# Kernel optimization log

Hardware: AMD Instinct MI355X
Metric: run time of the kernel (lower is better)

## Reference

```python
import jax, jax.numpy as jnp
import numpy as np
from jax import lax

D = 768; H = 8; DQ = D // H; NL = 6; FF = 3072; MAXREL = 100; NOUT = 1024
B = 8; T = 4096; CIN = 8
EPS = 1e-5
NREL = 2 * MAXREL - 1  # 199 learned relative positions, rel in [-99, 99]


def conv1d(x, w, b, stride=1, pad=1):
    # x [B,C,T], w [O,I,K]
    y = lax.conv_general_dilated(x, w, (stride,), [(pad, pad)],
                                 dimension_numbers=('NCH', 'OIH', 'NCH'))
    return y + b[None, :, None]


def bnorm(x, p):
    # eval-mode BatchNorm1d; p [4,C] = (gamma, beta, running_mean, running_var)
    g, be, m, v = p[0], p[1], p[2], p[3]
    return g[None, :, None] * (x - m[None, :, None]) * lax.rsqrt(v[None, :, None] + EPS) + be[None, :, None]


def resblock(x, c1w, c1b, b1, c2w, c2b, b2, rw, rb, br):
    h = jax.nn.relu(bnorm(conv1d(x, c1w, c1b, stride=2), b1))
    h = bnorm(conv1d(h, c2w, c2b), b2)
    res = bnorm(conv1d(x, rw, rb, stride=2, pad=0), br)
    return jax.nn.relu(h + res)


def layer_norm(x, g, b):
    mu = jnp.mean(x, axis=-1, keepdims=True)
    var = jnp.mean(jnp.square(x - mu), axis=-1, keepdims=True)
    return g * (x - mu) * lax.rsqrt(var + EPS) + b


def attention(x, wq, wk, wv, wo, rel):
    # x [B,L,D]; wq/wk/wv [H,D,DQ]; wo [H,DQ,D]; rel [H,NREL,DQ]
    L = x.shape[1]
    q = jnp.einsum('bld,hdk->bhlk', x, wq)
    k = jnp.einsum('bld,hdk->bhlk', x, wk)
    v = jnp.einsum('bld,hdk->bhlk', x, wv)
    logits = jnp.einsum('bhqk,bhmk->bhqm', q, k) / np.float32(np.sqrt(DQ))
    # relative positional logits: pos[b,h,i,j] = q[b,h,i] . rel[h, (j-i)+99] if |j-i|<100 else -1e8
    rel_logits = jnp.einsum('bhlk,hmk->bhlm', q, rel)  # [B,H,L,NREL]
    pos_idx = jnp.arange(L)[None, :] - jnp.arange(L)[:, None] + (MAXREL - 1)  # j - i + 99
    valid = (pos_idx >= 0) & (pos_idx < NREL)
    idxc = jnp.clip(pos_idx, 0, NREL - 1)
    pos = jnp.take_along_axis(rel_logits, idxc[None, None, :, :], axis=3)  # [B,H,L,L]
    logits = logits + jnp.where(valid[None, None], pos, jnp.float32(-1e8))
    probs = jax.nn.softmax(logits, axis=-1)
    o = jnp.einsum('bhqm,bhmk->bhqk', probs, v)
    return jnp.einsum('bhlk,hkd->bld', o, wo)


def forward(x_raw, rb1_c1w, rb1_c1b, rb1_bn1, rb1_c2w, rb1_c2b, rb1_bn2, rb1_rw, rb1_rb, rb1_bnr,
            rb23_c1w, rb23_c1b, rb23_bn1, rb23_c2w, rb23_c2b, rb23_bn2, rb23_rw, rb23_rb, rb23_bnr,
            w_in_w, w_in_b, wq, wk, wv, wo, rel_emb, ln1_g, ln1_b, ln2_g, ln2_b,
            ff1_w, ff1_b, ff2_w, ff2_b, w_out_w, w_out_b):
    x = jnp.transpose(x_raw, (0, 2, 1))  # [B, 8, T]
    x = resblock(x, rb1_c1w, rb1_c1b, rb1_bn1, rb1_c2w, rb1_c2b, rb1_bn2, rb1_rw, rb1_rb, rb1_bnr)
    for i in range(2):
        x = resblock(x, rb23_c1w[i], rb23_c1b[i], rb23_bn1[i], rb23_c2w[i], rb23_c2b[i],
                     rb23_bn2[i], rb23_rw[i], rb23_rb[i], rb23_bnr[i])
    x = jnp.transpose(x, (0, 2, 1))  # [B, L=T/8, D]
    x = x @ w_in_w.T + w_in_b
    for l in range(NL):  # post-norm transformer encoder layers
        x = layer_norm(x + attention(x, wq[l], wk[l], wv[l], wo[l], rel_emb[l]), ln1_g[l], ln1_b[l])
        h = jax.nn.relu(x @ ff1_w[l].T + ff1_b[l]) @ ff2_w[l].T + ff2_b[l]
        x = layer_norm(x + h, ln2_g[l], ln2_b[l])
    return x @ w_out_w.T + w_out_b


def setup_inputs() -> dict:
    key = jax.random.key(0)
    ks = iter(jax.random.split(key, 128))

    def w(shape, scale):
        return jax.random.normal(next(ks), shape, dtype=jnp.float32) * scale

    def bnp(*lead):
        g = 1.0 + 0.1 * jax.random.normal(next(ks), (*lead, D), dtype=jnp.float32)
        be = 0.1 * jax.random.normal(next(ks), (*lead, D), dtype=jnp.float32)
        m = 0.1 * jax.random.normal(next(ks), (*lead, D), dtype=jnp.float32)
        v = jax.random.uniform(next(ks), (*lead, D), minval=0.5, maxval=1.5, dtype=jnp.float32)
        return jnp.stack([g, be, m, v], axis=-2)  # [..., 4, D]

    inp = {}
    inp['x_raw'] = jax.random.normal(next(ks), (B, T, CIN), dtype=jnp.float32)
    inp['rb1_c1w'] = w((D, CIN, 3), 0.2); inp['rb1_c1b'] = w((D,), 0.02); inp['rb1_bn1'] = bnp()
    inp['rb1_c2w'] = w((D, D, 3), 0.02); inp['rb1_c2b'] = w((D,), 0.02); inp['rb1_bn2'] = bnp()
    inp['rb1_rw'] = w((D, CIN, 1), 0.2); inp['rb1_rb'] = w((D,), 0.02); inp['rb1_bnr'] = bnp()
    inp['rb23_c1w'] = w((2, D, D, 3), 0.02); inp['rb23_c1b'] = w((2, D), 0.02); inp['rb23_bn1'] = bnp(2)
    inp['rb23_c2w'] = w((2, D, D, 3), 0.02); inp['rb23_c2b'] = w((2, D), 0.02); inp['rb23_bn2'] = bnp(2)
    inp['rb23_rw'] = w((2, D, D, 1), 0.02); inp['rb23_rb'] = w((2, D), 0.02); inp['rb23_bnr'] = bnp(2)
    inp['w_in_w'] = w((D, D), 0.02); inp['w_in_b'] = w((D,), 0.02)
    sd = D ** -0.5
    inp['wq'] = w((NL, H, D, DQ), sd); inp['wk'] = w((NL, H, D, DQ), sd)
    inp['wv'] = w((NL, H, D, DQ), sd); inp['wo'] = w((NL, H, DQ, D), sd)
    inp['rel_emb'] = w((NL, H, NREL, DQ), DQ ** -0.5)
    inp['ln1_g'] = jnp.ones((NL, D), jnp.float32); inp['ln1_b'] = jnp.zeros((NL, D), jnp.float32)
    inp['ln2_g'] = jnp.ones((NL, D), jnp.float32); inp['ln2_b'] = jnp.zeros((NL, D), jnp.float32)
    inp['ff1_w'] = w((NL, FF, D), 0.02); inp['ff1_b'] = w((NL, FF), 0.02)
    inp['ff2_w'] = w((NL, D, FF), 0.02); inp['ff2_b'] = w((NL, D), 0.02)
    inp['w_out_w'] = w((NOUT, D), 0.02); inp['w_out_b'] = w((NOUT,), 0.02)
    return inp


def reference(x_raw, rb1_c1w, rb1_c1b, rb1_bn1, rb1_c2w, rb1_c2b, rb1_bn2, rb1_rw, rb1_rb, rb1_bnr,
              rb23_c1w, rb23_c1b, rb23_bn1, rb23_c2w, rb23_c2b, rb23_bn2, rb23_rw, rb23_rb, rb23_bnr,
              w_in_w, w_in_b, wq, wk, wv, wo, rel_emb, ln1_g, ln1_b, ln2_g, ln2_b,
              ff1_w, ff1_b, ff2_w, ff2_b, w_out_w, w_out_b):
    return forward(x_raw, rb1_c1w, rb1_c1b, rb1_bn1, rb1_c2w, rb1_c2b, rb1_bn2, rb1_rw, rb1_rb, rb1_bnr,
                   rb23_c1w, rb23_c1b, rb23_bn1, rb23_c2w, rb23_c2b, rb23_bn2, rb23_rw, rb23_rb, rb23_bnr,
                   w_in_w, w_in_b, wq, wk, wv, wo, rel_emb, ln1_g, ln1_b, ln2_g, ln2_b,
                   ff1_w, ff1_b, ff2_w, ff2_b, w_out_w, w_out_b)
```

## Files before the change

### kernel.cpp

```cpp
#include <hip/hip_runtime.h>
#include <math.h>

typedef __bf16 bf16;
typedef bf16 bf16x8 __attribute__((ext_vector_type(8)));
typedef bf16 bf16x4 __attribute__((ext_vector_type(4)));
typedef float f32x4 __attribute__((ext_vector_type(4)));
#define EPSF 1e-5f

__device__ __forceinline__ void ldg_lds16(const bf16* g, bf16* l) {
    __builtin_amdgcn_global_load_lds((const __attribute__((address_space(1))) void*)g,
                                     (__attribute__((address_space(3))) void*)l, 16, 0, 0);
}

__device__ __forceinline__ int xcd_swz(int orig, int nwg) {
    int xcd = orig & 7, base = orig >> 3;
    int q = nwg >> 3, r = nwg & 7;
    return (xcd < r ? xcd * (q + 1) : r * (q + 1) + (xcd - r) * q) + base;
}

template<bool BIAS, bool RESF, bool RELU, bool WF, bool WB, bool BAND>
__global__ __launch_bounds__(256) void mgemm_k(
    const bf16* __restrict__ A, const bf16* __restrict__ B,
    const float* __restrict__ bias, const float* __restrict__ resf,
    float* __restrict__ Cf, bf16* __restrict__ Cb,
    int K, int lda, int ldb, int ldc, int Nstore,
    int Z2, long long sA1, long long sA2, long long sB1, long long sB2,
    long long sC1, long long sC2)
{
    int z = blockIdx.z;
    int z1 = z / Z2, z2 = z - z1 * Z2;
    A += z1 * sA1 + z2 * sA2;
    B += z1 * sB1 + z2 * sB2;
    long long coff = z1 * sC1 + z2 * sC2;

    int bx = blockIdx.x, by = blockIdx.y;
    int nwg = gridDim.x * gridDim.y;
    if ((nwg & 7) == 0 && nwg >= 16) {
        int id = xcd_swz(by * gridDim.x + bx, nwg);
        bx = id % gridDim.x; by = id / gridDim.x;
    }

    __shared__ __align__(16) bf16 As[8192];
    __shared__ __align__(16) bf16 Bs[8192];
    int tid = threadIdx.x, wid = tid >> 6, lane = tid & 63;
    int m0 = by * 128, n0 = bx * 128;
    int wr = wid >> 1, wc = wid & 1;
    int lrow = lane & 15, lk8 = (lane >> 4) * 8;
    int srow = wid * 32 + (lane >> 2);
    int scol = (lane & 3) * 8;
    f32x4 acc[4][4] = {};

    int ktlo = 0, nt;
    if (BAND) {
        int lo = m0 - 99; if (lo < 0) lo = 0;
        ktlo = (lo >> 5) << 5;
        int hi = ((m0 + 226) >> 5) * 32 + 32;
        if (hi > K) hi = K;
        nt = (hi - ktlo) >> 5;
    } else {
        nt = K >> 5;
    }

#define STAGE_AB(cur, kt) do { \
    ldg_lds16(A + (size_t)(m0 + srow) * lda + (kt) + scol, As + (cur) * 4096 + wid * 1024); \
    ldg_lds16(A + (size_t)(m0 + srow + 16) * lda + (kt) + scol, As + (cur) * 4096 + wid * 1024 + 512); \
    ldg_lds16(B + (size_t)(n0 + srow) * ldb + (kt) + scol, Bs + (cur) * 4096 + wid * 1024); \
    ldg_lds16(B + (size_t)(n0 + srow + 16) * ldb + (kt) + scol, Bs + (cur) * 4096 + wid * 1024 + 512); \
} while (0)

    STAGE_AB(0, ktlo);
    __syncthreads();
    for (int t = 0; t < nt; t++) {
        int cur = t & 1;
        if (t + 1 < nt) STAGE_AB(cur ^ 1, ktlo + (t + 1) * 32);
        bf16x8 af[4], bfr[4];
#pragma unroll
        for (int i = 0; i < 4; i++) {
            af[i]  = *(const bf16x8*)(As + cur * 4096 + (wr * 64 + i * 16 + lrow) * 32 + lk8);
            bfr[i] = *(const bf16x8*)(Bs + cur * 4096 + (wc * 64 + i * 16 + lrow) * 32 + lk8);
        }
#pragma unroll
        for (int i = 0; i < 4; i++)
#pragma unroll
            for (int j = 0; j < 4; j++)
                acc[i][j] = __builtin_amdgcn_mfma_f32_16x16x32_bf16(af[i], bfr[j], acc[i][j], 0, 0, 0);
        __syncthreads();
    }
#undef STAGE_AB

    int mtop = m0 + wr * 64 + (lane >> 4) * 4;
    int ntop = n0 + wc * 64 + lrow;
#pragma unroll
    for (int mi = 0; mi < 4; mi++) {
#pragma unroll
        for (int r = 0; r < 4; r++) {
            int m = mtop + mi * 16 + r;
            long long ro = coff + (long long)m * ldc;
#pragma unroll
            for (int ni = 0; ni < 4; ni++) {
                int n = ntop + ni * 16;
                float v = acc[mi][ni][r];
                if (BIAS) v += bias[n];
                if (RESF) v += resf[ro + n];
                if (RELU) v = fmaxf(v, 0.f);
                if (n < Nstore) {
                    if (WF) Cf[ro + n] = v;
                    if (WB) Cb[ro + n] = (bf16)v;
                }
            }
        }
    }
}

template<bool RES, bool RELU>
__global__ __launch_bounds__(256) void conv_k(
    const bf16* __restrict__ in, const bf16* __restrict__ w,
    const float* __restrict__ scsh, const bf16* __restrict__ res, bf16* __restrict__ out,
    int KK, int stride, int rowoff, long long instrideB, long long outstrideB, int outoff,
    long long resstrideB)
{
    int z = blockIdx.z;
    int bx = blockIdx.x, by = blockIdx.y;
    int nwg = gridDim.x * gridDim.y;
    if ((nwg & 7) == 0 && nwg >= 16) {
        int id = xcd_swz(by * gridDim.x + bx, nwg);
        bx = id % gridDim.x; by = id / gridDim.x;
    }
    int n0 = bx * 128, m0 = by * 128;
    __shared__ __align__(16) bf16 As[8192];
    __shared__ __align__(16) bf16 Bs[8192];
    int tid = threadIdx.x, wid = tid >> 6, lane = tid & 63;
    int wr = wid >> 1, wc = wid & 1;
    int lrow = lane & 15, lk8 = (lane >> 4) * 8;
    int srow = wid * 32 + (lane >> 2);
    int scol = (lane & 3) * 8;
    const bf16* inz = in + (size_t)z * instrideB;
    f32x4 acc[4][4] = {};
    int nt = KK >> 5;

#define STAGE_CV(cur, kt) do { \
    int kq_ = (kt) / 768; \
    int ic0_ = (kt) - kq_ * 768; \
    ldg_lds16(inz + (size_t)((m0 + srow) * stride + kq_ + rowoff) * 768 + ic0_ + scol, As + (cur) * 4096 + wid * 1024); \
    ldg_lds16(inz + (size_t)((m0 + srow + 16) * stride + kq_ + rowoff) * 768 + ic0_ + scol, As + (cur) * 4096 + wid * 1024 + 512); \
    ldg_lds16(w + (size_t)(n0 + srow) * KK + (kt) + scol, Bs + (cur) * 4096 + wid * 1024); \
    ldg_lds16(w + (size_t)(n0 + srow + 16) * KK + (kt) + scol, Bs + (cur) * 4096 + wid * 1024 + 512); \
} while (0)

    STAGE_CV(0, 0);
    __syncthreads();
    for (int t = 0; t < nt; t++) {
        int cur = t & 1;
        if (t + 1 < nt) STAGE_CV(cur ^ 1, (t + 1) * 32);
        bf16x8 af[4], bfr[4];
#pragma unroll
        for (int i = 0; i < 4; i++) {
            af[i]  = *(const bf16x8*)(As + cur * 4096 + (wr * 64 + i * 16 + lrow) * 32 + lk8);
            bfr[i] = *(const bf16x8*)(Bs + cur * 4096 + (wc * 64 + i * 16 + lrow) * 32 + lk8);
        }
#pragma unroll
        for (int i = 0; i < 4; i++)
#pragma unroll
            for (int j = 0; j < 4; j++)
                acc[i][j] = __builtin_amdgcn_mfma_f32_16x16x32_bf16(af[i], bfr[j], acc[i][j], 0, 0, 0);
        __syncthreads();
    }
#undef STAGE_CV

    bf16* outz = out + (size_t)z * outstrideB + (size_t)outoff * 768;
    const bf16* resz = res + (RES ? (size_t)z * resstrideB : 0);
    int mtop = m0 + wr * 64 + (lane >> 4) * 4;
    int ntop = n0 + wc * 64 + lrow;
#pragma unroll
    for (int mi = 0; mi < 4; mi++) {
#pragma unroll
        for (int r = 0; r < 4; r++) {
            int m = mtop + mi * 16 + r;
#pragma unroll
            for (int ni = 0; ni < 4; ni++) {
                int n = ntop + ni * 16;
                float v = acc[mi][ni][r] * scsh[n] + scsh[768 + n];
                if (RES) v += (float)resz[(size_t)m * 768 + n];
                if (RELU) v = fmaxf(v, 0.f);
                outz[(size_t)m * 768 + n] = (bf16)v;
            }
        }
    }
}

__device__ const int qk_ti[10] = {0, 0, 1, 1, 1, 2, 2, 2, 3, 3};
__device__ const int qk_tj[10] = {0, 1, 0, 1, 2, 1, 2, 3, 2, 3};

__global__ __launch_bounds__(256) void qkrel_k(
    const bf16* __restrict__ qkv, const float* __restrict__ relb, float* __restrict__ lg)
{
    int z = blockIdx.z, b = z >> 3, h = z & 7;
    int i0 = qk_ti[blockIdx.x] * 128, j0 = qk_tj[blockIdx.x] * 128;
    long long lgbase = (long long)z * 262144;
    const bf16* Aq = qkv + (size_t)b * 512 * 2304 + h * 96;
    const bf16* Bk = Aq + 768;
    __shared__ __align__(16) bf16 As[8192];
    __shared__ __align__(16) bf16 Bs[8192];
    int tid = threadIdx.x, wid = tid >> 6, lane = tid & 63;
    int wr = wid >> 1, wc = wid & 1;
    int lrow = lane & 15, lk8 = (lane >> 4) * 8;
    int srow = wid * 32 + (lane >> 2);
    int scol = (lane & 3) * 8;
    f32x4 acc[4][4] = {};

#define STAGE_QK(cur, kt) do { \
    ldg_lds16(Aq + (size_t)(i0 + srow) * 2304 + (kt) + scol, As + (cur) * 4096 + wid * 1024); \
    ldg_lds16(Aq + (size_t)(i0 + srow + 16) * 2304 + (kt) + scol, As + (cur) * 4096 + wid * 1024 + 512); \
    ldg_lds16(Bk + (size_t)(j0 + srow) * 2304 + (kt) + scol, Bs + (cur) * 4096 + wid * 1024); \
    ldg_lds16(Bk + (size_t)(j0 + srow + 16) * 2304 + (kt) + scol, Bs + (cur) * 4096 + wid * 1024 + 512); \
} while (0)

    STAGE_QK(0, 0);
    __syncthreads();
    for (int t = 0; t < 3; t++) {
        int cur = t & 1;
        if (t + 1 < 3) STAGE_QK(cur ^ 1, (t + 1) * 32);
        bf16x8 af[4], bfr[4];
#pragma unroll
        for (int i = 0; i < 4; i++) {
            af[i]  = *(const bf16x8*)(As + cur * 4096 + (wr * 64 + i * 16 + lrow) * 32 + lk8);
            bfr[i] = *(const bf16x8*)(Bs + cur * 4096 + (wc * 64 + i * 16 + lrow) * 32 + lk8);
        }
#pragma unroll
        for (int i = 0; i < 4; i++)
#pragma unroll
            for (int j = 0; j < 4; j++)
                acc[i][j] = __builtin_amdgcn_mfma_f32_16x16x32_bf16(af[i], bfr[j], acc[i][j], 0, 0, 0);
        __syncthreads();
    }
#undef STAGE_QK

    const float sc = 0.10206207261596577f;
    int itop = i0 + wr * 64 + (lane >> 4) * 4;
    int jtop = j0 + wc * 64 + lrow;
#pragma unroll
    for (int mi = 0; mi < 4; mi++) {
#pragma unroll
        for (int r = 0; r < 4; r++) {
            int i = itop + mi * 16 + r;
            const float* rrow = relb + ((long long)h * 4096 + b * 512 + i) * 256;
#pragma unroll
            for (int ni = 0; ni < 4; ni++) {
                int j = jtop + ni * 16;
                float v = acc[mi][ni][r] * sc;
                int idx = j - i + 99;
                v += (idx >= 0 && idx < 199) ? rrow[idx] : -1e8f;
                lg[lgbase + (long long)i * 512 + j] = v;
            }
        }
    }
}

__global__ __launch_bounds__(256) void softmax_k(float* __restrict__ lg)
{
    __shared__ float red1[4];
    __shared__ float red2[4];
    size_t r = blockIdx.x;
    int i = (int)(r & 511);
    int jlo = i - 99; if (jlo < 0) jlo = 0;
    int jhi = i + 100; if (jhi > 512) jhi = 512;
    float* p = lg + r * 512;
    int tid = threadIdx.x;
    int j = jlo + tid;
    bool act = j < jhi;
    float v = act ? p[j] : -1e30f;
    float m = v;
#pragma unroll
    for (int off = 32; off; off >>= 1) m = fmaxf(m, __shfl_xor(m, off));
    if ((tid & 63) == 0) red1[tid >> 6] = m;
    __syncthreads();
    m = fmaxf(fmaxf(red1[0], red1[1]), fmaxf(red1[2], red1[3]));
    float e = act ? expf(v - m) : 0.f;
    float s = e;
#pragma unroll
    for (int off = 32; off; off >>= 1) s += __shfl_xor(s, off);
    if ((tid & 63) == 0) red2[tid >> 6] = s;
    __syncthreads();
    float inv = 1.f / (red2[0] + red2[1] + red2[2] + red2[3]);
    bf16* pb = (bf16*)p;
    if (act) pb[j] = (bf16)(e * inv);
#pragma unroll
    for (int c = tid; c < 512; c += 256)
        if (c < jlo || c >= jhi) pb[c] = (bf16)0.f;
}

__global__ __launch_bounds__(256) void ln2_k(const float* __restrict__ in,
                                             const float* __restrict__ g,
                                             const float* __restrict__ b,
                                             float* __restrict__ xf, bf16* __restrict__ xb)
{
    __shared__ float red1[4];
    __shared__ float red2[4];
    int r = blockIdx.x, tid = threadIdx.x;
    const float* p = in + (size_t)r * 768;
    float x0 = p[tid], x1 = p[tid + 256], x2 = p[tid + 512];
    float s = x0 + x1 + x2;
#pragma unroll
    for (int off = 32; off; off >>= 1) s += __shfl_xor(s, off);
    if ((tid & 63) == 0) red1[tid >> 6] = s;
    __syncthreads();
    float mu = (red1[0] + red1[1] + red1[2] + red1[3]) * (1.f / 768.f);
    float d0 = x0 - mu, d1 = x1 - mu, d2 = x2 - mu;
    float sq = d0 * d0 + d1 * d1 + d2 * d2;
#pragma unroll
    for (int off = 32; off; off >>= 1) sq += __shfl_xor(sq, off);
    if ((tid & 63) == 0) red2[tid >> 6] = sq;
    __syncthreads();
    float rstd = rsqrtf((red2[0] + red2[1] + red2[2] + red2[3]) * (1.f / 768.f) + EPSF);
    float o0 = g[tid] * d0 * rstd + b[tid];
    float o1 = g[tid + 256] * d1 * rstd + b[tid + 256];
    float o2 = g[tid + 512] * d2 * rstd + b[tid + 512];
    size_t base = (size_t)r * 768;
    xf[base + tid] = o0;       xb[base + tid] = (bf16)o0;
    xf[base + tid + 256] = o1; xb[base + tid + 256] = (bf16)o1;
    xf[base + tid + 512] = o2; xb[base + tid + 512] = (bf16)o2;
}

__global__ __launch_bounds__(256) void rb1_front_k(
    const float* __restrict__ xr, const float* __restrict__ c1w, const float* __restrict__ rw,
    const float* __restrict__ scsh0, const float* __restrict__ scsh1,
    bf16* __restrict__ h1, bf16* __restrict__ res1)
{
    int t = blockIdx.x, b = blockIdx.y, tid = threadIdx.x;
    const float* xb = xr + (size_t)b * 4096 * 8;
    float xv[3][8];
#pragma unroll
    for (int k = 0; k < 3; k++) {
        int pos = 2 * t + k - 1;
        bool ok = (unsigned)pos < 4096u;
        const float* xp = xb + (size_t)pos * 8;
#pragma unroll
        for (int c = 0; c < 8; c++) xv[k][c] = ok ? xp[c] : 0.f;
    }
#pragma unroll
    for (int rep = 0; rep < 3; rep++) {
        int o = rep * 256 + tid;
        float conv = 0.f;
        const float* wp = c1w + (size_t)o * 24;
#pragma unroll
        for (int c = 0; c < 8; c++)
#pragma unroll
            for (int k = 0; k < 3; k++) conv = fmaf(wp[c * 3 + k], xv[k][c], conv);
        float hv = fmaxf(conv * scsh0[o] + scsh0[768 + o], 0.f);
        h1[((size_t)b * 2050 + t + 1) * 768 + o] = (bf16)hv;
        float cr = 0.f;
        const float* rp = rw + (size_t)o * 8;
#pragma unroll
        for (int c = 0; c < 8; c++) cr = fmaf(rp[c], xv[1][c], cr);
        res1[((size_t)b * 2048 + t) * 768 + o] = (bf16)(cr * scsh1[o] + scsh1[768 + o]);
    }
}

__global__ void bnprep_k(const float* __restrict__ bn, const float* __restrict__ cb,
                         float* __restrict__ scsh)
{
    int i = blockIdx.x * 256 + threadIdx.x;
    if (i >= 768) return;
    float g = bn[i], be = bn[768 + i], m = bn[1536 + i], v = bn[2304 + i];
    float sc = g * rsqrtf(v + EPSF);
    scsh[i] = sc;
    scsh[768 + i] = (cb[i] - m) * sc + be;
}

__global__ void zeropad_k(bf16* __restrict__ buf, int T)
{
    int i = blockIdx.x * 256 + threadIdx.x;
    if (i >= 768) return;
    int row = blockIdx.y ? (T + 1) : 0;
    buf[((size_t)blockIdx.z * (T + 2) + row) * 768 + i] = (bf16)0.f;
}

__global__ void rep3_k(const float* __restrict__ w, bf16* __restrict__ wr)
{
    long long i = (long long)blockIdx.x * 256 + threadIdx.x;
    if (i >= 1769472) return;
    int o = i / 2304, k = i - (long long)o * 2304;
    int kq = k / 768, ic = k - kq * 768;
    wr[i] = (bf16)w[((long long)o * 768 + ic) * 3 + kq];
}

__global__ void cast4_k(const float* __restrict__ s, bf16* __restrict__ d, int n4)
{
    int i = blockIdx.x * 256 + threadIdx.x;
    if (i >= n4) return;
    float4 v = ((const float4*)s)[i];
    bf16x4 o = {(bf16)v.x, (bf16)v.y, (bf16)v.z, (bf16)v.w};
    ((bf16x4*)d)[i] = o;
}

__global__ void layerprep_k(const float* __restrict__ wq, const float* __restrict__ wk,
                            const float* __restrict__ wv, const float* __restrict__ wo,
                            const float* __restrict__ rel,
                            const float* __restrict__ ff1, const float* __restrict__ ff2,
                            bf16* __restrict__ Wqkv, bf16* __restrict__ Wo,
                            bf16* __restrict__ Rel, bf16* __restrict__ F1, bf16* __restrict__ F2)
{
    long long i = (long long)blockIdx.x * 256 + threadIdx.x;
    const long long S0 = 1769472, S1 = 589824, S2 = 196608, S3 = 2359296;
    if (i < S0) {
        int n = i / 768, k = i - (long long)n * 768;
        int sel = n / 768, hq = n - sel * 768;
        int h = hq / 96, q = hq - h * 96;
        const float* src = sel == 0 ? wq : (sel == 1 ? wk : wv);
        Wqkv[i] = (bf16)src[((long long)h * 768 + k) * 96 + q];
    } else if (i < S0 + S1) {
        long long j = i - S0;
        int n = j / 768, kk = j - (long long)n * 768;
        Wo[j] = (bf16)wo[(long long)kk * 768 + n];
    } else if (i < S0 + S1 + S2) {
        long long j = i - S0 - S1;
        int h = j / 24576, rest = j - (long long)h * 24576;
        int rr = rest / 96, q = rest - rr * 96;
        Rel[j] = rr < 199 ? (bf16)rel[((long long)h * 199 + rr) * 96 + q] : (bf16)0.f;
    } else if (i < S0 + S1 + S2 + S3) {
        long long j = i - S0 - S1 - S2;
        F1[j] = (bf16)ff1[j];
    } else {
        long long j = i - S0 - S1 - S2 - S3;
        F2[j] = (bf16)ff2[j];
    }
}

__global__ __launch_bounds__(256) void vt_k(const bf16* __restrict__ qkv, bf16* __restrict__ vt)
{
    int z = blockIdx.z, b = z >> 3, h = z & 7;
    int t0 = blockIdx.x * 32, q0 = blockIdx.y * 32;
    __shared__ bf16 sm[32][33];
    int tx = threadIdx.x & 31, ty = threadIdx.x >> 5;
#pragma unroll
    for (int s = 0; s < 4; s++) {
        int t = t0 + ty + s * 8, q = q0 + tx;
        sm[ty + s * 8][tx] = (q < 96) ? qkv[((size_t)b * 512 + t) * 2304 + 1536 + h * 96 + q]
                                      : (bf16)0.f;
    }
    __syncthreads();
#pragma unroll
    for (int s = 0; s < 4; s++) {
        int q = q0 + ty + s * 8;
        vt[((size_t)z * 128 + q) * 512 + t0 + tx] = sm[tx][ty + s * 8];
    }
}

extern "C" void kernel_launch(void* const* d_in, const int* in_sizes, int n_in,
                              void* d_out, int out_size, void* d_ws, size_t ws_size,
                              hipStream_t stream)
{
    const float* x_raw    = (const float*)d_in[0];
    const float* rb1_c1w  = (const float*)d_in[1];
    const float* rb1_c1b  = (const float*)d_in[2];
    const float* rb1_bn1  = (const float*)d_in[3];
    const float* rb1_c2w  = (const float*)d_in[4];
    const float* rb1_c2b  = (const float*)d_in[5];
    const float* rb1_bn2  = (const float*)d_in[6];
    const float* rb1_rw   = (const float*)d_in[7];
    const float* rb1_rb   = (const float*)d_in[8];
    const float* rb1_bnr  = (const float*)d_in[9];
    const float* rb23_c1w = (const float*)d_in[10];
    const float* rb23_c1b = (const float*)d_in[11];
    const float* rb23_bn1 = (const float*)d_in[12];
    const float* rb23_c2w = (const float*)d_in[13];
    const float* rb23_c2b = (const float*)d_in[14];
    const float* rb23_bn2 = (const float*)d_in[15];
    const float* rb23_rw  = (const float*)d_in[16];
    const float* rb23_rb  = (const float*)d_in[17];
    const float* rb23_bnr = (const float*)d_in[18];
    const float* w_in_w   = (const float*)d_in[19];
    const float* w_in_b   = (const float*)d_in[20];
    const float* wq       = (const float*)d_in[21];
    const float* wk       = (const float*)d_in[22];
    const float* wv       = (const float*)d_in[23];
    const float* wo       = (const float*)d_in[24];
    const float* rel_emb  = (const float*)d_in[25];
    const float* ln1_g    = (const float*)d_in[26];
    const float* ln1_b    = (const float*)d_in[27];
    const float* ln2_g    = (const float*)d_in[28];
    const float* ln2_b    = (const float*)d_in[29];
    const float* ff1_w    = (const float*)d_in[30];
    const float* ff1_b    = (const float*)d_in[31];
    const float* ff2_w    = (const float*)d_in[32];
    const float* ff2_b    = (const float*)d_in[33];
    const float* w_out_w  = (const float*)d_in[34];
    const float* w_out_b  = (const float*)d_in[35];
    float* out = (float*)d_out;

    char* W = (char*)d_ws;
    bf16*  h1buf  = (bf16*)(W + 0);
    bf16*  resbuf = (bf16*)(W + 26000000);
    bf16*  xbuf   = (bf16*)(W + 52000000);
    float* lg     = (float*)(W + 0);
    bf16*  wc3    = (bf16*)(W + 78000000);
    bf16*  wc1    = (bf16*)(W + 82000000);
    float* scsh   = (float*)(W + 84000000);
    float* xf     = (float*)(W + 85000000);
    bf16*  xb     = (bf16*)(W + 98000000);
    bf16*  qkv    = (bf16*)(W + 105000000);
    bf16*  vt     = (bf16*)(W + 124000000);
    float* relb   = (float*)(W + 133000000);
    bf16*  ffh    = (bf16*)(W + 133000000);
    bf16*  atno   = (bf16*)(W + 167000000);
    float* tmp    = (float*)(W + 174000000);
    bf16*  Wqkv   = (bf16*)(W + 187000000);
    bf16*  Wo     = (bf16*)(W + 191000000);
    bf16*  F1     = (bf16*)(W + 193000000);
    bf16*  F2     = (bf16*)(W + 198000000);
    bf16*  Relp   = (bf16*)(W + 203000000);
    bf16*  Wout   = (bf16*)(W + 204000000);
    bf16*  Winw   = (bf16*)(W + 206000000);

    bnprep_k<<<3, 256, 0, stream>>>(rb1_bn1, rb1_c1b, scsh + 0 * 1536);
    bnprep_k<<<3, 256, 0, stream>>>(rb1_bnr, rb1_rb,  scsh + 1 * 1536);
    bnprep_k<<<3, 256, 0, stream>>>(rb1_bn2, rb1_c2b, scsh + 2 * 1536);
    bnprep_k<<<3, 256, 0, stream>>>(rb23_bn1, rb23_c1b, scsh + 3 * 1536);
    bnprep_k<<<3, 256, 0, stream>>>(rb23_bnr, rb23_rb,  scsh + 4 * 1536);
    bnprep_k<<<3, 256, 0, stream>>>(rb23_bn2, rb23_c2b, scsh + 5 * 1536);
    bnprep_k<<<3, 256, 0, stream>>>(rb23_bn1 + 3072, rb23_c1b + 768, scsh + 6 * 1536);
    bnprep_k<<<3, 256, 0, stream>>>(rb23_bnr + 3072, rb23_rb + 768,  scsh + 7 * 1536);
    bnprep_k<<<3, 256, 0, stream>>>(rb23_bn2 + 3072, rb23_c2b + 768, scsh + 8 * 1536);

    rb1_front_k<<<dim3(2048, 8), 256, 0, stream>>>(x_raw, rb1_c1w, rb1_rw,
                                                   scsh, scsh + 1536, h1buf, resbuf);
    zeropad_k<<<dim3(3, 2, 8), 256, 0, stream>>>(h1buf, 2048);
    rep3_k<<<6912, 256, 0, stream>>>(rb1_c2w, wc3);
    conv_k<true, true><<<dim3(6, 16, 8), 256, 0, stream>>>(
        h1buf, wc3, scsh + 2 * 1536, resbuf, xbuf, 2304, 1, 0,
        (long long)2050 * 768, (long long)2050 * 768, 1, (long long)2048 * 768);
    zeropad_k<<<dim3(3, 2, 8), 256, 0, stream>>>(xbuf, 2048);
    rep3_k<<<6912, 256, 0, stream>>>(rb23_c1w, wc3);
    conv_k<false, true><<<dim3(6, 8, 8), 256, 0, stream>>>(
        xbuf, wc3, scsh + 3 * 1536, nullptr, h1buf, 2304, 2, 0,
        (long long)2050 * 768, (long long)1026 * 768, 1, 0);
    zeropad_k<<<dim3(3, 2, 8), 256, 0, stream>>>(h1buf, 1024);
    cast4_k<<<576, 256, 0, stream>>>(rb23_rw, wc1, 147456);
    conv_k<false, false><<<dim3(6, 8, 8), 256, 0, stream>>>(
        xbuf, wc1, scsh + 4 * 1536, nullptr, resbuf, 768, 2, 1,
        (long long)2050 * 768, (long long)1024 * 768, 0, 0);
    rep3_k<<<6912, 256, 0, stream>>>(rb23_c2w, wc3);
    conv_k<true, true><<<dim3(6, 8, 8), 256, 0, stream>>>(
        h1buf, wc3, scsh + 5 * 1536, resbuf, xbuf, 2304, 1, 0,
        (long long)1026 * 768, (long long)1026 * 768, 1, (long long)1024 * 768);
    zeropad_k<<<dim3(3, 2, 8), 256, 0, stream>>>(xbuf, 1024);
    rep3_k<<<6912, 256, 0, stream>>>(rb23_c1w + 1769472, wc3);
    conv_k<false, true><<<dim3(6, 4, 8), 256, 0, stream>>>(
        xbuf, wc3, scsh + 6 * 1536, nullptr, h1buf, 2304, 2, 0,
        (long long)1026 * 768, (long long)514 * 768, 1, 0);
    zeropad_k<<<dim3(3, 2, 8), 256, 0, stream>>>(h1buf, 512);
    cast4_k<<<576, 256, 0, stream>>>(rb23_rw + 589824, wc1, 147456);
    conv_k<false, false><<<dim3(6, 4, 8), 256, 0, stream>>>(
        xbuf, wc1, scsh + 7 * 1536, nullptr, resbuf, 768, 2, 1,
        (long long)1026 * 768, (long long)512 * 768, 0, 0);
    rep3_k<<<6912, 256, 0, stream>>>(rb23_c2w + 1769472, wc3);
    conv_k<true, true><<<dim3(6, 4, 8), 256, 0, stream>>>(
        h1buf, wc3, scsh + 8 * 1536, resbuf, xbuf, 2304, 1, 0,
        (long long)514 * 768, (long long)512 * 768, 0, (long long)512 * 768);

    cast4_k<<<576, 256, 0, stream>>>(w_in_w, Winw, 147456);
    cast4_k<<<768, 256, 0, stream>>>(w_out_w, Wout, 196608);
    mgemm_k<true, false, false, true, true, false><<<dim3(6, 32, 1), 256, 0, stream>>>(
        xbuf, Winw, w_in_b, nullptr, xf, xb, 768, 768, 768, 768, 768, 1, 0, 0, 0, 0, 0, 0);

    for (int l = 0; l < 6; l++) {
        layerprep_k<<<28416, 256, 0, stream>>>(
            wq + (size_t)l * 589824, wk + (size_t)l * 589824, wv + (size_t)l * 589824,
            wo + (size_t)l * 589824, rel_emb + (size_t)l * 152832,
            ff1_w + (size_t)l * 2359296, ff2_w + (size_t)l * 2359296,
            Wqkv, Wo, Relp, F1, F2);
        mgemm_k<false, false, false, false, true, false><<<dim3(18, 32, 1), 256, 0, stream>>>(
            xb, Wqkv, nullptr, nullptr, nullptr, qkv, 768, 768, 768, 2304, 2304,
            1, 0, 0, 0, 0, 0, 0);
        vt_k<<<dim3(16, 4, 64), 256, 0, stream>>>(qkv, vt);
        mgemm_k<false, false, false, true, false, false><<<dim3(2, 32, 8), 256, 0, stream>>>(
            qkv, Relp, nullptr, nullptr, relb, nullptr, 96, 2304, 96, 256, 256,
            1, 96, 0, 24576, 0, 1048576, 0);
        qkrel_k<<<dim3(10, 1, 64), 256, 0, stream>>>(qkv, relb, lg);
        softmax_k<<<32768, 256, 0, stream>>>(lg);
        mgemm_k<false, false, false, false, true, true><<<dim3(1, 4, 64), 256, 0, stream>>>(
            (const bf16*)lg, vt, nullptr, nullptr, nullptr, atno, 512, 1024, 512, 768, 96,
            8, 4194304, 524288, 524288, 65536, 393216, 96);
        mgemm_k<false, true, false, true, false, false><<<dim3(6, 32, 1), 256, 0, stream>>>(
            atno, Wo, nullptr, xf, tmp, nullptr, 768, 768, 768, 768, 768,
            1, 0, 0, 0, 0, 0, 0);
        ln2_k<<<4096, 256, 0, stream>>>(tmp, ln1_g + l * 768, ln1_b + l * 768, xf, xb);
        mgemm_k<true, false, true, false, true, false><<<dim3(24, 32, 1), 256, 0, stream>>>(
            xb, F1, ff1_b + l * 3072, nullptr, nullptr, ffh, 768, 768, 768, 3072, 3072,
            1, 0, 0, 0, 0, 0, 0);
        mgemm_k<true, true, false, true, false, false><<<dim3(6, 32, 1), 256, 0, stream>>>(
            ffh, F2, ff2_b + l * 768, xf, tmp, nullptr, 3072, 3072, 3072, 768, 768,
            1, 0, 0, 0, 0, 0, 0);
        ln2_k<<<4096, 256, 0, stream>>>(tmp, ln2_g + l * 768, ln2_b + l * 768, xf, xb);
    }

    mgemm_k<true, false, false, true, false, false><<<dim3(8, 32, 1), 256, 0, stream>>>(
        xb, Wout, w_out_b, nullptr, out, nullptr, 768, 768, 768, 1024, 1024,
        1, 0, 0, 0, 0, 0, 0);
}
```

Baseline: 2.591 ms.

## Split-K with atomics for narrow GEMMs, MFMA front conv, merged prep kernels

The Wo, FF2 and output GEMMs now use split-K across blockIdx.z and accumulate into zero-initialised fp32 buffers with atomicAdd. The LayerNorm kernel re-zeroes tmp after reading it so the next split-K pass starts from zero. The scalar first-resblock front conv is replaced by a padded bf16 MFMA GEMM that fuses the conv and residual paths. The nine BN-prep launches are merged into one, and zero-padding moves into the conv kernels. The aim is to fill more CUs on the 192-block GEMMs and cut launch overhead, at the cost of atomic traffic, extra zero-fill passes and nondeterministic summation order.

Result: no change. 2.587 ms (-0.2%).

```diff
diff --git a/kernel.cpp b/kernel.cpp
--- a/kernel.cpp
+++ b/kernel.cpp
@@ -18,16 +18,17 @@
     return (xcd < r ? xcd * (q + 1) : r * (q + 1) + (xcd - r) * q) + base;
 }
 
-template<bool BIAS, bool RESF, bool RELU, bool WF, bool WB, bool BAND>
+template<bool BIAS, bool RESF, bool RELU, bool WF, bool WB, bool BAND, bool ATOM = false>
 __global__ __launch_bounds__(256) void mgemm_k(
     const bf16* __restrict__ A, const bf16* __restrict__ B,
     const float* __restrict__ bias, const float* __restrict__ resf,
     float* __restrict__ Cf, bf16* __restrict__ Cb,
     int K, int lda, int ldb, int ldc, int Nstore,
     int Z2, long long sA1, long long sA2, long long sB1, long long sB2,
-    long long sC1, long long sC2)
-{
-    int z = blockIdx.z;
+    long long sC1, long long sC2, int kchunks)
+{
+    int z = blockIdx.z, kc = 0;
+    if (ATOM) { kc = z % kchunks; z /= kchunks; }
     int z1 = z / Z2, z2 = z - z1 * Z2;
     A += z1 * sA1 + z2 * sA2;
     B += z1 * sB1 + z2 * sB2;
@@ -50,7 +51,8 @@
     int scol = (lane & 3) * 8;
     f32x4 acc[4][4] = {};
 
-    int ktlo = 0, nt;
+    int Klen = ATOM ? (K / kchunks) : K;
+    int ktlo, nt;
     if (BAND) {
         int lo = m0 - 99; if (lo < 0) lo = 0;
         ktlo = (lo >> 5) << 5;
@@ -58,7 +60,8 @@
         if (hi > K) hi = K;
         nt = (hi - ktlo) >> 5;
     } else {
-        nt = K >> 5;
+        ktlo = ATOM ? kc * Klen : 0;
+        nt = Klen >> 5;
     }
 
 #define STAGE_AB(cur, kt) do { \
@@ -100,11 +103,11 @@
             for (int ni = 0; ni < 4; ni++) {
                 int n = ntop + ni * 16;
                 float v = acc[mi][ni][r];
-                if (BIAS) v += bias[n];
-                if (RESF) v += resf[ro + n];
+                if (BIAS && (!ATOM || kc == 0)) v += bias[n];
+                if (RESF && (!ATOM || kc == 0)) v += resf[ro + n];
                 if (RELU) v = fmaxf(v, 0.f);
                 if (n < Nstore) {
-                    if (WF) Cf[ro + n] = v;
+                    if (WF) { if (ATOM) atomicAdd(&Cf[ro + n], v); else Cf[ro + n] = v; }
                     if (WB) Cb[ro + n] = (bf16)v;
                 }
             }
@@ -117,7 +120,7 @@
     const bf16* __restrict__ in, const bf16* __restrict__ w,
     const float* __restrict__ scsh, const bf16* __restrict__ res, bf16* __restrict__ out,
     int KK, int stride, int rowoff, long long instrideB, long long outstrideB, int outoff,
-    long long resstrideB)
+    long long resstrideB, int padT)
 {
     int z = blockIdx.z;
     int bx = blockIdx.x, by = blockIdx.y;
@@ -138,6 +141,14 @@
     f32x4 acc[4][4] = {};
     int nt = KK >> 5;
 
+    if (padT && blockIdx.x == 0 && blockIdx.y == 0) {
+        bf16* pz = out + (size_t)z * outstrideB;
+        for (int i = tid; i < 768; i += 256) {
+            pz[i] = (bf16)0.f;
+            pz[(size_t)(padT + 1) * 768 + i] = (bf16)0.f;
+        }
+    }
+
 #define STAGE_CV(cur, kt) do { \
     int kq_ = (kt) / 768; \
     int ic0_ = (kt) - kq_ * 768; \
@@ -183,6 +194,72 @@
                 if (RES) v += (float)resz[(size_t)m * 768 + n];
                 if (RELU) v = fmaxf(v, 0.f);
                 outz[(size_t)m * 768 + n] = (bf16)v;
+            }
+        }
+    }
+}
+
+__global__ __launch_bounds__(256) void rb1gemm_k(
+    const bf16* __restrict__ xpadb, const bf16* __restrict__ Wrb1,
+    const float* __restrict__ scsh0, const float* __restrict__ scshR,
+    bf16* __restrict__ h1, bf16* __restrict__ res1)
+{
+    int b = blockIdx.z;
+    int n0 = blockIdx.x * 128, m0 = blockIdx.y * 128;
+    __shared__ __align__(16) bf16 As[4096];
+    __shared__ __align__(16) bf16 Bs[4096];
+    int tid = threadIdx.x, wid = tid >> 6, lane = tid & 63;
+    int wr = wid >> 1, wc = wid & 1;
+    int lrow = lane & 15, lk8 = (lane >> 4) * 8;
+    int srow = wid * 32 + (lane >> 2);
+    int scol = (lane & 3) * 8;
+
+    if (blockIdx.x == 0 && blockIdx.y == 0) {
+        bf16* pz = h1 + (size_t)b * 2050 * 768;
+        for (int i = tid; i < 768; i += 256) {
+            pz[i] = (bf16)0.f;
+            pz[(size_t)2049 * 768 + i] = (bf16)0.f;
+        }
+    }
+
+    const bf16* xb = xpadb + (size_t)b * 32800;
+    ldg_lds16(xb + (size_t)(m0 + srow) * 16 + scol, As + wid * 1024);
+    ldg_lds16(xb + (size_t)(m0 + srow + 16) * 16 + scol, As + wid * 1024 + 512);
+    ldg_lds16(Wrb1 + (size_t)(n0 + srow) * 32 + scol, Bs + wid * 1024);
+    ldg_lds16(Wrb1 + (size_t)(n0 + srow + 16) * 32 + scol, Bs + wid * 1024 + 512);
+    __syncthreads();
+    f32x4 acc[4][4] = {};
+    bf16x8 af[4], bfr[4];
+#pragma unroll
+    for (int i = 0; i < 4; i++) {
+        af[i]  = *(const bf16x8*)(As + (wr * 64 + i * 16 + lrow) * 32 + lk8);
+        bfr[i] = *(const bf16x8*)(Bs + (wc * 64 + i * 16 + lrow) * 32 + lk8);
+    }
+#pragma unroll
+    for (int i = 0; i < 4; i++)
+#pragma unroll
+        for (int j = 0; j < 4; j++)
+            acc[i][j] = __builtin_amdgcn_mfma_f32_16x16x32_bf16(af[i], bfr[j], acc[i][j], 0, 0, 0);
+
+    int mtop = m0 + wr * 64 + (lane >> 4) * 4;
+    int ntop = n0 + wc * 64 + lrow;
+#pragma unroll
+    for (int mi = 0; mi < 4; mi++) {
+#pragma unroll
+        for (int r = 0; r < 4; r++) {
+            int m = mtop + mi * 16 + r;
+#pragma unroll
+            for (int ni = 0; ni < 4; ni++) {
+                int n = ntop + ni * 16;
+                float a = acc[mi][ni][r];
+                if (n < 768) {
+                    float v = fmaxf(a * scsh0[n] + scsh0[768 + n], 0.f);
+                    h1[((size_t)b * 2050 + m + 1) * 768 + n] = (bf16)v;
+                } else {
+                    int o = n - 768;
+                    float v = a * scshR[o] + scshR[768 + o];
+                    res1[((size_t)b * 2048 + m) * 768 + o] = (bf16)v;
+                }
             }
         }
     }
@@ -289,7 +366,7 @@
         if (c < jlo || c >= jhi) pb[c] = (bf16)0.f;
 }
 
-__global__ __launch_bounds__(256) void ln2_k(const float* __restrict__ in,
+__global__ __launch_bounds__(256) void ln2_k(float* tmp,
                                              const float* __restrict__ g,
                                              const float* __restrict__ b,
                                              float* __restrict__ xf, bf16* __restrict__ xb)
@@ -297,7 +374,7 @@
     __shared__ float red1[4];
     __shared__ float red2[4];
     int r = blockIdx.x, tid = threadIdx.x;
-    const float* p = in + (size_t)r * 768;
+    float* p = tmp + (size_t)r * 768;
     float x0 = p[tid], x1 = p[tid + 256], x2 = p[tid + 512];
     float s = x0 + x1 + x2;
 #pragma unroll
@@ -315,64 +392,55 @@
     float o0 = g[tid] * d0 * rstd + b[tid];
     float o1 = g[tid + 256] * d1 * rstd + b[tid + 256];
     float o2 = g[tid + 512] * d2 * rstd + b[tid + 512];
+    p[tid] = 0.f; p[tid + 256] = 0.f; p[tid + 512] = 0.f;
     size_t base = (size_t)r * 768;
     xf[base + tid] = o0;       xb[base + tid] = (bf16)o0;
     xf[base + tid + 256] = o1; xb[base + tid + 256] = (bf16)o1;
     xf[base + tid + 512] = o2; xb[base + tid + 512] = (bf16)o2;
 }
 
-__global__ __launch_bounds__(256) void rb1_front_k(
-    const float* __restrict__ xr, const float* __restrict__ c1w, const float* __restrict__ rw,
-    const float* __restrict__ scsh0, const float* __restrict__ scsh1,
-    bf16* __restrict__ h1, bf16* __restrict__ res1)
-{
-    int t = blockIdx.x, b = blockIdx.y, tid = threadIdx.x;
-    const float* xb = xr + (size_t)b * 4096 * 8;
-    float xv[3][8];
-#pragma unroll
-    for (int k = 0; k < 3; k++) {
-        int pos = 2 * t + k - 1;
-        bool ok = (unsigned)pos < 4096u;
-        const float* xp = xb + (size_t)pos * 8;
-#pragma unroll
-        for (int c = 0; c < 8; c++) xv[k][c] = ok ? xp[c] : 0.f;
-    }
-#pragma unroll
-    for (int rep = 0; rep < 3; rep++) {
-        int o = rep * 256 + tid;
-        float conv = 0.f;
-        const float* wp = c1w + (size_t)o * 24;
-#pragma unroll
-        for (int c = 0; c < 8; c++)
-#pragma unroll
-            for (int k = 0; k < 3; k++) conv = fmaf(wp[c * 3 + k], xv[k][c], conv);
-        float hv = fmaxf(conv * scsh0[o] + scsh0[768 + o], 0.f);
-        h1[((size_t)b * 2050 + t + 1) * 768 + o] = (bf16)hv;
-        float cr = 0.f;
-        const float* rp = rw + (size_t)o * 8;
-#pragma unroll
-        for (int c = 0; c < 8; c++) cr = fmaf(rp[c], xv[1][c], cr);
-        res1[((size_t)b * 2048 + t) * 768 + o] = (bf16)(cr * scsh1[o] + scsh1[768 + o]);
-    }
-}
-
-__global__ void bnprep_k(const float* __restrict__ bn, const float* __restrict__ cb,
-                         float* __restrict__ scsh)
-{
+struct BnPtrs { const float* bn[9]; const float* cb[9]; };
+__global__ void bnprep9_k(BnPtrs p, float* __restrict__ scsh)
+{
+    int slot = blockIdx.y;
     int i = blockIdx.x * 256 + threadIdx.x;
     if (i >= 768) return;
+    const float* bn = p.bn[slot];
     float g = bn[i], be = bn[768 + i], m = bn[1536 + i], v = bn[2304 + i];
     float sc = g * rsqrtf(v + EPSF);
-    scsh[i] = sc;
-    scsh[768 + i] = (cb[i] - m) * sc + be;
-}
-
-__global__ void zeropad_k(bf16* __restrict__ buf, int T)
+    scsh[slot * 1536 + i] = sc;
+    scsh[slot * 1536 + 768 + i] = (p.cb[slot][i] - m) * sc + be;
+}
+
+__global__ void zerof_k(float* __restrict__ p, long long n4)
+{
+    long long i = (long long)blockIdx.x * 256 + threadIdx.x;
+    long long stride = (long long)gridDim.x * 256;
+    float4 z = make_float4(0.f, 0.f, 0.f, 0.f);
+    for (; i < n4; i += stride) ((float4*)p)[i] = z;
+}
+
+__global__ void xprep_k(const float* __restrict__ xr, bf16* __restrict__ xpadb)
 {
     int i = blockIdx.x * 256 + threadIdx.x;
-    if (i >= 768) return;
-    int row = blockIdx.y ? (T + 1) : 0;
-    buf[((size_t)blockIdx.z * (T + 2) + row) * 768 + i] = (bf16)0.f;
+    if (i >= 262400) return;
+    int c = i & 7, rb_ = i >> 3;
+    int r = rb_ % 4100, b = rb_ / 4100;
+    float v = (r >= 1 && r <= 4096) ? xr[((size_t)b * 4096 + r - 1) * 8 + c] : 0.f;
+    xpadb[i] = (bf16)v;
+}
+
+__global__ void rb1wprep_k(const float* __restrict__ c1w, const float* __restrict__ rw,
+                           bf16* __restrict__ Wrb1)
+{
+    int i = blockIdx.x * 256 + threadIdx.x;
+    if (i >= 49152) return;
+    int n = i >> 5, k = i & 31;
+    int kq = k >> 3, c = k & 7;
+    float v = 0.f;
+    if (n < 768) { if (kq < 3) v = c1w[((size_t)n * 8 + c) * 3 + kq]; }
+    else         { if (kq == 1) v = rw[(size_t)(n - 768) * 8 + c]; }
+    Wrb1[i] = (bf16)v;
 }
 
 __global__ void rep3_k(const float* __restrict__ w, bf16* __restrict__ wr)
@@ -495,6 +563,8 @@
     float* lg     = (float*)(W + 0);
     bf16*  wc3    = (bf16*)(W + 78000000);
     bf16*  wc1    = (bf16*)(W + 82000000);
+    bf16*  xpadb  = (bf16*)(W + 83300000);
+    bf16*  Wrb1   = (bf16*)(W + 83900000);
     float* scsh   = (float*)(W + 84000000);
     float* xf     = (float*)(W + 85000000);
     bf16*  xb     = (bf16*)(W + 98000000);
@@ -512,56 +582,57 @@
     bf16*  Wout   = (bf16*)(W + 204000000);
     bf16*  Winw   = (bf16*)(W + 206000000);
 
-    bnprep_k<<<3, 256, 0, stream>>>(rb1_bn1, rb1_c1b, scsh + 0 * 1536);
-    bnprep_k<<<3, 256, 0, stream>>>(rb1_bnr, rb1_rb,  scsh + 1 * 1536);
-    bnprep_k<<<3, 256, 0, stream>>>(rb1_bn2, rb1_c2b, scsh + 2 * 1536);
-    bnprep_k<<<3, 256, 0, stream>>>(rb23_bn1, rb23_c1b, scsh + 3 * 1536);
-    bnprep_k<<<3, 256, 0, stream>>>(rb23_bnr, rb23_rb,  scsh + 4 * 1536);
-    bnprep_k<<<3, 256, 0, stream>>>(rb23_bn2, rb23_c2b, scsh + 5 * 1536);
-    bnprep_k<<<3, 256, 0, stream>>>(rb23_bn1 + 3072, rb23_c1b + 768, scsh + 6 * 1536);
-    bnprep_k<<<3, 256, 0, stream>>>(rb23_bnr + 3072, rb23_rb + 768,  scsh + 7 * 1536);
-    bnprep_k<<<3, 256, 0, stream>>>(rb23_bn2 + 3072, rb23_c2b + 768, scsh + 8 * 1536);
-
-    rb1_front_k<<<dim3(2048, 8), 256, 0, stream>>>(x_raw, rb1_c1w, rb1_rw,
-                                                   scsh, scsh + 1536, h1buf, resbuf);
-    zeropad_k<<<dim3(3, 2, 8), 256, 0, stream>>>(h1buf, 2048);
+    BnPtrs bp;
+    bp.bn[0] = rb1_bn1; bp.cb[0] = rb1_c1b;
+    bp.bn[1] = rb1_bnr; bp.cb[1] = rb1_rb;
+    bp.bn[2] = rb1_bn2; bp.cb[2] = rb1_c2b;
+    bp.bn[3] = rb23_bn1; bp.cb[3] = rb23_c1b;
+    bp.bn[4] = rb23_bnr; bp.cb[4] = rb23_rb;
+    bp.bn[5] = rb23_bn2; bp.cb[5] = rb23_c2b;
+    bp.bn[6] = rb23_bn1 + 3072; bp.cb[6] = rb23_c1b + 768;
+    bp.bn[7] = rb23_bnr + 3072; bp.cb[7] = rb23_rb + 768;
+    bp.bn[8] = rb23_bn2 + 3072; bp.cb[8] = rb23_c2b + 768;
+    bnprep9_k<<<dim3(3, 9), 256, 0, stream>>>(bp, scsh);
+
+    xprep_k<<<1025, 256, 0, stream>>>(x_raw, xpadb);
+    rb1wprep_k<<<192, 256, 0, stream>>>(rb1_c1w, rb1_rw, Wrb1);
+    rb1gemm_k<<<dim3(12, 16, 8), 256, 0, stream>>>(xpadb, Wrb1, scsh, scsh + 1536, h1buf, resbuf);
+
     rep3_k<<<6912, 256, 0, stream>>>(rb1_c2w, wc3);
     conv_k<true, true><<<dim3(6, 16, 8), 256, 0, stream>>>(
         h1buf, wc3, scsh + 2 * 1536, resbuf, xbuf, 2304, 1, 0,
-        (long long)2050 * 768, (long long)2050 * 768, 1, (long long)2048 * 768);
-    zeropad_k<<<dim3(3, 2, 8), 256, 0, stream>>>(xbuf, 2048);
+        (long long)2050 * 768, (long long)2050 * 768, 1, (long long)2048 * 768, 2048);
     rep3_k<<<6912, 256, 0, stream>>>(rb23_c1w, wc3);
     conv_k<false, true><<<dim3(6, 8, 8), 256, 0, stream>>>(
         xbuf, wc3, scsh + 3 * 1536, nullptr, h1buf, 2304, 2, 0,
-        (long long)2050 * 768, (long long)1026 * 768, 1, 0);
-    zeropad_k<<<dim3(3, 2, 8), 256, 0, stream>>>(h1buf, 1024);
+        (long long)2050 * 768, (long long)1026 * 768, 1, 0, 1024);
     cast4_k<<<576, 256, 0, stream>>>(rb23_rw, wc1, 147456);
     conv_k<false, false><<<dim3(6, 8, 8), 256, 0, stream>>>(
         xbuf, wc1, scsh + 4 * 1536, nullptr, resbuf, 768, 2, 1,
-        (long long)2050 * 768, (long long)1024 * 768, 0, 0);
+        (long long)2050 * 768, (long long)1024 * 768, 0, 0, 0);
     rep3_k<<<6912, 256, 0, stream>>>(rb23_c2w, wc3);
     conv_k<true, true><<<dim3(6, 8, 8), 256, 0, stream>>>(
         h1buf, wc3, scsh + 5 * 1536, resbuf, xbuf, 2304, 1, 0,
-        (long long)1026 * 768, (long long)1026 * 768, 1, (long long)1024 * 768);
-    zeropad_k<<<dim3(3, 2, 8), 256, 0, stream>>>(xbuf, 1024);
+        (long long)1026 * 768, (long long)1026 * 768, 1, (long long)1024 * 768, 1024);
     rep3_k<<<6912, 256, 0, stream>>>(rb23_c1w + 1769472, wc3);
     conv_k<false, true><<<dim3(6, 4, 8), 256, 0, stream>>>(
         xbuf, wc3, scsh + 6 * 1536, nullptr, h1buf, 2304, 2, 0,
-        (long long)1026 * 768, (long long)514 * 768, 1, 0);
-    zeropad_k<<<dim3(3, 2, 8), 256, 0, stream>>>(h1buf, 512);
+        (long long)1026 * 768, (long long)514 * 768, 1, 0, 512);
     cast4_k<<<576, 256, 0, stream>>>(rb23_rw + 589824, wc1, 147456);
     conv_k<false, false><<<dim3(6, 4, 8), 256, 0, stream>>>(
         xbuf, wc1, scsh + 7 * 1536, nullptr, resbuf, 768, 2, 1,
-        (long long)1026 * 768, (long long)512 * 768, 0, 0);
+        (long long)1026 * 768, (long long)512 * 768, 0, 0, 0);
     rep3_k<<<6912, 256, 0, stream>>>(rb23_c2w + 1769472, wc3);
     conv_k<true, true><<<dim3(6, 4, 8), 256, 0, stream>>>(
         h1buf, wc3, scsh + 8 * 1536, resbuf, xbuf, 2304, 1, 0,
-        (long long)514 * 768, (long long)512 * 768, 0, (long long)512 * 768);
+        (long long)514 * 768, (long long)512 * 768, 0, (long long)512 * 768, 0);
 
     cast4_k<<<576, 256, 0, stream>>>(w_in_w, Winw, 147456);
     cast4_k<<<768, 256, 0, stream>>>(w_out_w, Wout, 196608);
+    zerof_k<<<2048, 256, 0, stream>>>(tmp, 786432);
     mgemm_k<true, false, false, true, true, false><<<dim3(6, 32, 1), 256, 0, stream>>>(
-        xbuf, Winw, w_in_b, nullptr, xf, xb, 768, 768, 768, 768, 768, 1, 0, 0, 0, 0, 0, 0);
+        xbuf, Winw, w_in_b, nullptr, xf, xb, 768, 768, 768, 768, 768,
+        1, 0, 0, 0, 0, 0, 0, 1);
 
     for (int l = 0; l < 6; l++) {
         layerprep_k<<<28416, 256, 0, stream>>>(
@@ -571,30 +642,31 @@
             Wqkv, Wo, Relp, F1, F2);
         mgemm_k<false, false, false, false, true, false><<<dim3(18, 32, 1), 256, 0, stream>>>(
             xb, Wqkv, nullptr, nullptr, nullptr, qkv, 768, 768, 768, 2304, 2304,
-            1, 0, 0, 0, 0, 0, 0);
+            1, 0, 0, 0, 0, 0, 0, 1);
         vt_k<<<dim3(16, 4, 64), 256, 0, stream>>>(qkv, vt);
         mgemm_k<false, false, false, true, false, false><<<dim3(2, 32, 8), 256, 0, stream>>>(
             qkv, Relp, nullptr, nullptr, relb, nullptr, 96, 2304, 96, 256, 256,
-            1, 96, 0, 24576, 0, 1048576, 0);
+            1, 96, 0, 24576, 0, 1048576, 0, 1);
         qkrel_k<<<dim3(10, 1, 64), 256, 0, stream>>>(qkv, relb, lg);
         softmax_k<<<32768, 256, 0, stream>>>(lg);
         mgemm_k<false, false, false, false, true, true><<<dim3(1, 4, 64), 256, 0, stream>>>(
             (const bf16*)lg, vt, nullptr, nullptr, nullptr, atno, 512, 1024, 512, 768, 96,
-            8, 4194304, 524288, 524288, 65536, 393216, 96);
-        mgemm_k<false, true, false, true, false, false><<<dim3(6, 32, 1), 256, 0, stream>>>(
+            8, 4194304, 524288, 524288, 65536, 393216, 96, 1);
+        mgemm_k<false, true, false, true, false, false, true><<<dim3(6, 32, 2), 256, 0, stream>>>(
             atno, Wo, nullptr, xf, tmp, nullptr, 768, 768, 768, 768, 768,
-            1, 0, 0, 0, 0, 0, 0);
+            1, 0, 0, 0, 0, 0, 0, 2);
         ln2_k<<<4096, 256, 0, stream>>>(tmp, ln1_g + l * 768, ln1_b + l * 768, xf, xb);
         mgemm_k<true, false, true, false, true, false><<<dim3(24, 32, 1), 256, 0, stream>>>(
             xb, F1, ff1_b + l * 3072, nullptr, nullptr, ffh, 768, 768, 768, 3072, 3072,
-            1, 0, 0, 0, 0, 0, 0);
-        mgemm_k<true, true, false, true, false, false><<<dim3(6, 32, 1), 256, 0, stream>>>(
+            1, 0, 0, 0, 0, 0, 0, 1);
+        mgemm_k<true, true, false, true, false, false, true><<<dim3(6, 32, 4), 256, 0, stream>>>(
             ffh, F2, ff2_b + l * 768, xf, tmp, nullptr, 3072, 3072, 3072, 768, 768,
-            1, 0, 0, 0, 0, 0, 0);
+            1, 0, 0, 0, 0, 0, 0, 4);
         ln2_k<<<4096, 256, 0, stream>>>(tmp, ln2_g + l * 768, ln2_b + l * 768, xf, xb);
     }
 
-    mgemm_k<true, false, false, true, false, false><<<dim3(8, 32, 1), 256, 0, stream>>>(
+    zerof_k<<<2048, 256, 0, stream>>>(out, 1048576);
+    mgemm_k<true, false, false, true, false, false, true><<<dim3(8, 32, 2), 256, 0, stream>>>(
         xb, Wout, w_out_b, nullptr, out, nullptr, 768, 768, 768, 1024, 1024,
-        1, 0, 0, 0, 0, 0, 0);
-}
+        1, 0, 0, 0, 0, 0, 0, 2);
+}
```
